# Performance work log

Hardware: AMD Instinct MI355X
Metric: run time of the kernel (lower is better)

## Reference

```python
import jax, jax.numpy as jnp
import numpy as np

B, NPG, DEG = 512, 128, 16          # graphs, nodes/graph, out-degree
N = B * NPG                          # 65536 nodes
E = N * DEG                          # 1048576 edges
IN_DIM, HID, HEADS = 11, 32, 4
K1 = int(np.ceil(0.8 * NPG))         # 103 nodes/graph after pool1
K2 = int(np.ceil(0.8 * K1))          # 83 nodes/graph after pool2


def gat_conv(x, src, dst, mask, W, a_s, a_d, b, n_nodes):
    # PyG GATConv (concat=True, add_self_loops=True, eval mode -> no dropout)
    xp = (x @ W).reshape(n_nodes, HEADS, HID)            # [N,H,C]
    as_ = jnp.einsum('nhc,hc->nh', xp, a_s)
    ad_ = jnp.einsum('nhc,hc->nh', xp, a_d)
    loop = jnp.arange(n_nodes)
    s = jnp.concatenate([src, loop])
    d = jnp.concatenate([dst, loop])
    m = jnp.concatenate([mask, jnp.ones(n_nodes, bool)])
    logit = jax.nn.leaky_relu(as_[s] + ad_[d], 0.2)      # [E+N,H]
    logit = jnp.where(m[:, None], logit, -1e9)
    mx = jax.ops.segment_max(logit, d, num_segments=n_nodes)
    ex = jnp.exp(logit - mx[d]) * m[:, None]
    den = jax.ops.segment_sum(ex, d, num_segments=n_nodes)
    alpha = ex / (den[d] + 1e-16)                        # segment softmax over dst
    out = jax.ops.segment_sum(alpha[:, :, None] * xp[s], d, num_segments=n_nodes)
    return out.reshape(n_nodes, HEADS * HID) + b


def topk_pool(x, src, dst, mask, w, npg, k):
    # PyG TopKPooling: score = tanh((x*w).sum(-1)/||w||); keep top ceil(ratio*n) per graph
    nb = x.shape[0] // npg
    score = jnp.tanh((x @ w) / jnp.linalg.norm(w))
    vals, idx = jax.lax.top_k(score.reshape(nb, npg), k)  # [B,k]
    perm = (idx + (jnp.arange(nb) * npg)[:, None]).reshape(-1)
    x_new = x[perm] * vals.reshape(-1, 1)
    remap = jnp.full(nb * npg, -1).at[perm].set(jnp.arange(nb * k))
    ns, nd = remap[src], remap[dst]
    m = mask & (ns >= 0) & (nd >= 0)
    return x_new, jnp.where(m, ns, 0), jnp.where(m, nd, 0), m


def setup_inputs():
    key = jax.random.key(0)
    ks = jax.random.split(key, 24)
    s = 0.05
    x = jax.random.normal(ks[0], (N, IN_DIM), jnp.float32)
    src = jnp.repeat(jnp.arange(N), DEG)
    dst = (src // NPG) * NPG + jax.random.randint(ks[1], (E,), 0, NPG)
    edge_index = jnp.stack([src, dst])
    edge_attr = jax.random.normal(ks[2], (E, 4), jnp.float32)
    batch = jnp.repeat(jnp.arange(B), NPG)
    p = dict(
        W_g1=jax.random.normal(ks[3], (IN_DIM, HEADS * HID), jnp.float32) * s,
        att_src1=jax.random.normal(ks[4], (HEADS, HID), jnp.float32) * s,
        att_dst1=jax.random.normal(ks[5], (HEADS, HID), jnp.float32) * s,
        b_g1=jnp.zeros((HEADS * HID,), jnp.float32),
        W_t1=jax.random.normal(ks[6], (HEADS * HID, HID), jnp.float32) * s,
        b_t1=jnp.zeros((HID,), jnp.float32),
        pool_w1=jax.random.normal(ks[7], (HID,), jnp.float32) * s,
        W_g2=jax.random.normal(ks[8], (HID, HEADS * HID), jnp.float32) * s,
        att_src2=jax.random.normal(ks[9], (HEADS, HID), jnp.float32) * s,
        att_dst2=jax.random.normal(ks[10], (HEADS, HID), jnp.float32) * s,
        b_g2=jnp.zeros((HEADS * HID,), jnp.float32),
        W_t2=jax.random.normal(ks[11], (HEADS * HID, HID), jnp.float32) * s,
        b_t2=jnp.zeros((HID,), jnp.float32),
        pool_w2=jax.random.normal(ks[12], (HID,), jnp.float32) * s,
        W_l1=jax.random.normal(ks[13], (2 * HID, 256), jnp.float32) * s,
        b_l1=jnp.zeros((256,), jnp.float32),
        W_l2=jax.random.normal(ks[14], (256, 1024), jnp.float32) * s,
        b_l2=jnp.zeros((1024,), jnp.float32),
        W_l3=jax.random.normal(ks[15], (1024, 1), jnp.float32) * s,
        b_l3=jnp.zeros((1,), jnp.float32),
    )
    return dict(x=x, edge_index=edge_index, edge_attr=edge_attr, batch=batch, **p)


def reference(x, edge_index, edge_attr, batch,
              W_g1, att_src1, att_dst1, b_g1, W_t1, b_t1, pool_w1,
              W_g2, att_src2, att_dst2, b_g2, W_t2, b_t2, pool_w2,
              W_l1, b_l1, W_l2, b_l2, W_l3, b_l3):
    # edge_attr is ignored (GATConv built without edge_dim); batch is implicit
    # in the fixed equal-size graph layout.  Eval mode -> dropout disabled.
    src, dst = edge_index[0], edge_index[1]
    mask = jnp.ones(E, bool)
    h = jax.nn.relu(gat_conv(x, src, dst, mask, W_g1, att_src1, att_dst1, b_g1, N))
    h = h @ W_t1 + b_t1
    h, src, dst, mask = topk_pool(h, src, dst, mask, pool_w1, NPG, K1)
    h1 = h.reshape(B, K1, HID)
    g1 = jnp.concatenate([h1.max(1), h1.mean(1)], axis=1)   # [B, 2*HID]
    h = jax.nn.relu(gat_conv(h, src, dst, mask, W_g2, att_src2, att_dst2, b_g2, B * K1))
    h = h @ W_t2 + b_t2
    h, src, dst, mask = topk_pool(h, src, dst, mask, pool_w2, K1, K2)
    h2 = h.reshape(B, K2, HID)
    g2 = jnp.concatenate([h2.max(1), h2.mean(1)], axis=1)
    g = g1 + g2
    g = jax.nn.relu(g @ W_l1 + b_l1)
    g = jax.nn.relu(g @ W_l2 + b_l2)
    return g @ W_l3 + b_l3                                   # [B,1]
```

## Files before the change

kernel.cpp:

```cpp
#include <hip/hip_runtime.h>
#include <math.h>

constexpr int NPGc  = 128;
constexpr int NG    = 512;
constexpr int EPGc  = 2048;
constexpr int ETOT  = 1048576;
constexpr int IND   = 11;
constexpr int HIDc  = 32;
constexpr int FD    = 128;
constexpr int K1c   = 103;
constexpr int K2c   = 83;
constexpr int NN    = NG * NPGc;
constexpr int N2c   = NG * K1c;
constexpr int EPAD  = 2432;
constexpr int SBCAP = 2560;
constexpr int OFFSTR= 264;

__device__ __forceinline__ float lrelu(float x){ return fmaxf(x, 0.2f*x); }

__device__ __forceinline__ void agg4(const float4* __restrict__ X4, int r, int cbase, float e,
                                     float4& A0, float4& A1, float4& A2, float4& A3)
{
    int b = r * 8, s = r & 7;
    float4 u0 = X4[b + ((cbase+0) ^ s)];
    A0.x = fmaf(e, u0.x, A0.x); A0.y = fmaf(e, u0.y, A0.y); A0.z = fmaf(e, u0.z, A0.z); A0.w = fmaf(e, u0.w, A0.w);
    float4 u1 = X4[b + ((cbase+1) ^ s)];
    A1.x = fmaf(e, u1.x, A1.x); A1.y = fmaf(e, u1.y, A1.y); A1.z = fmaf(e, u1.z, A1.z); A1.w = fmaf(e, u1.w, A1.w);
    float4 u2 = X4[b + ((cbase+2) ^ s)];
    A2.x = fmaf(e, u2.x, A2.x); A2.y = fmaf(e, u2.y, A2.y); A2.z = fmaf(e, u2.z, A2.z); A2.w = fmaf(e, u2.w, A2.w);
    float4 u3 = X4[b + ((cbase+3) ^ s)];
    A3.x = fmaf(e, u3.x, A3.x); A3.y = fmaf(e, u3.y, A3.y); A3.z = fmaf(e, u3.z, A3.z); A3.w = fmaf(e, u3.w, A3.w);
}

template<int KIN>
__device__ void foldDev(const float* __restrict__ Wg, const float* __restrict__ avs,
                        const float* __restrict__ avd, float* __restrict__ S, float* __restrict__ D, int t)
{
    if (t < KIN * 4) {
        int k = t >> 2, h = t & 3;
        float s = 0.f, d = 0.f;
        for (int j = 0; j < HIDc; j++) {
            float w = Wg[k*FD + h*HIDc + j];
            s = fmaf(w, avs[h*HIDc + j], s);
            d = fmaf(w, avd[h*HIDc + j], d);
        }
        S[t] = s; D[t] = d;
    }
}

__global__ __launch_bounds__(256) void k_prep(const int* __restrict__ ei,
    const float* __restrict__ W1g, const float* __restrict__ s1, const float* __restrict__ d1,
    const float* __restrict__ W2g, const float* __restrict__ s2, const float* __restrict__ d2,
    int* __restrict__ csrOff, unsigned char* __restrict__ csrSB,
    float* __restrict__ S1, float* __restrict__ D1, float* __restrict__ S2, float* __restrict__ D2)
{
    int b = blockIdx.x, t = threadIdx.x;
    if (b >= NG) {
        if (b == NG)     foldDev<IND>(W1g, s1, d1, S1, D1, t);
        else             foldDev<HIDc>(W2g, s2, d2, S2, D2, t);
        return;
    }
    int g = b;
    __shared__ int cnt[128], cur[128], offL[129];
    __shared__ __align__(16) unsigned char sbL[SBCAP];
    const int FILL1 = (int)0x80808080u;
    if (t < 128) cnt[t] = 0;
    if (t < SBCAP/16) ((int4*)sbL)[t] = make_int4(FILL1, FILL1, FILL1, FILL1);
    __syncthreads();
    const int* dstG = ei + ETOT + g * EPGc;
    int dnv[8];
    #pragma unroll
    for (int q = 0; q < 8; q++) {
        int e = t + 256*q;
        dnv[q] = dstG[e] - g * NPGc;
        atomicAdd(&cnt[dnv[q]], 1);
    }
    __syncthreads();
    if (t < 64) {
        int c0 = cnt[2*t], c1 = cnt[2*t + 1];
        int p0 = (c0 + 3) & ~3, p1 = (c1 + 3) & ~3;
        int ps = p0 + p1, P = ps;
        #pragma unroll
        for (int dl = 1; dl < 64; dl <<= 1) { int v = __shfl_up(P, dl); if (t >= dl) P += v; }
        int E0 = P - ps;
        offL[2*t] = E0; offL[2*t + 1] = E0 + p0;
        cur[2*t]  = E0; cur[2*t + 1]  = E0 + p0;
        if (t == 63) offL[128] = P;
    }
    __syncthreads();
    #pragma unroll
    for (int q = 0; q < 8; q++) {
        int e = t + 256*q;
        int pos = atomicAdd(&cur[dnv[q]], 1);
        sbL[pos] = (unsigned char)(e >> 4);
    }
    __syncthreads();
    if (t < SBCAP/16) ((int4*)(csrSB + (size_t)g * SBCAP))[t] = ((const int4*)sbL)[t];
    if (t <= 128) csrOff[g*OFFSTR + t] = offL[t];
    if (t < 128)  csrOff[g*OFFSTR + 132 + t] = cur[t];
}

template<int NNODE, int KIN>
__global__ __launch_bounds__(256) void k_gat(
    const float* __restrict__ xin, const float* __restrict__ Wg,
    const float* __restrict__ WsS, const float* __restrict__ WsD,
    const int* __restrict__ csrOff, const unsigned char* __restrict__ csrSB,
    const float* __restrict__ bias, const float* __restrict__ Wt,
    float* __restrict__ htp)
{
    int g = blockIdx.x, h = blockIdx.y, t = threadIdx.x;
    __shared__ __align__(16) float xpL[NNODE * 32];
    __shared__ __align__(16) float WL[KIN * 32];
    __shared__ __align__(16) unsigned char sbL[SBCAP];
    __shared__ float asL[NNODE + 1], adL[NNODE];
    __shared__ unsigned short offL[NNODE + 1];

    const float* xg = xin + (size_t)g * NNODE * KIN;

    for (int i = t; i < KIN * 32; i += 256) { int k = i >> 5, c = i & 31; WL[i] = Wg[k*FD + h*32 + c]; }
    if (t <= NNODE) offL[t] = (unsigned short)csrOff[g*OFFSTR + t];
    if (t < SBCAP/16) ((int4*)sbL)[t] = ((const int4*)(csrSB + (size_t)g * SBCAP))[t];
    if (t == 0) asL[NNODE] = -1e30f;
    __syncthreads();

    for (int p = t; p < NNODE * 8; p += 256) {
        int n = p >> 3, c4 = p & 7;
        float4 acc = make_float4(0.f, 0.f, 0.f, 0.f);
        if constexpr ((KIN & 3) == 0) {
            const float4* xr4 = (const float4*)(xg + (size_t)n * KIN);
            #pragma unroll
            for (int k4 = 0; k4 < KIN/4; k4++) {
                float4 xv = xr4[k4];
                float4 w;
                w = *(const float4*)&WL[(k4*4+0)*32 + c4*4];
                acc.x = fmaf(xv.x, w.x, acc.x); acc.y = fmaf(xv.x, w.y, acc.y); acc.z = fmaf(xv.x, w.z, acc.z); acc.w = fmaf(xv.x, w.w, acc.w);
                w = *(const float4*)&WL[(k4*4+1)*32 + c4*4];
                acc.x = fmaf(xv.y, w.x, acc.x); acc.y = fmaf(xv.y, w.y, acc.y); acc.z = fmaf(xv.y, w.z, acc.z); acc.w = fmaf(xv.y, w.w, acc.w);
                w = *(const float4*)&WL[(k4*4+2)*32 + c4*4];
                acc.x = fmaf(xv.z, w.x, acc.x); acc.y = fmaf(xv.z, w.y, acc.y); acc.z = fmaf(xv.z, w.z, acc.z); acc.w = fmaf(xv.z, w.w, acc.w);
                w = *(const float4*)&WL[(k4*4+3)*32 + c4*4];
                acc.x = fmaf(xv.w, w.x, acc.x); acc.y = fmaf(xv.w, w.y, acc.y); acc.z = fmaf(xv.w, w.z, acc.z); acc.w = fmaf(xv.w, w.w, acc.w);
            }
        } else {
            const float* xr = xg + (size_t)n * KIN;
            #pragma unroll
            for (int k = 0; k < KIN; k++) {
                float xv = xr[k];
                float4 w4 = *(const float4*)&WL[k*32 + c4*4];
                acc.x = fmaf(xv, w4.x, acc.x); acc.y = fmaf(xv, w4.y, acc.y);
                acc.z = fmaf(xv, w4.z, acc.z); acc.w = fmaf(xv, w4.w, acc.w);
            }
        }
        ((float4*)xpL)[n*8 + (c4 ^ (n & 7))] = acc;
    }
    if (t < NNODE) {
        const float* xr = xg + (size_t)t * KIN;
        float s = 0.f, d = 0.f;
        #pragma unroll
        for (int k = 0; k < KIN; k++) { float v = xr[k]; s = fmaf(v, WsS[k*4 + h], s); d = fmaf(v, WsD[k*4 + h], d); }
        asL[t] = s; adL[t] = d;
    }
    __syncthreads();

    const float4* X4 = (const float4*)xpL;
    float4 A0, A1, A2, A3;
    int n = 0, cbase = 0;
    bool act = (t < NNODE * 2);
    if (act) {
        n = t >> 1;
        const int half = t & 1;
        cbase = half * 4;
        float as_n = asL[n], adn = adL[n];
        int lo = offL[n], hi = offL[n + 1];
        int mid = lo + (((hi - lo) >> 3) << 2);
        int slo = half ? mid : lo;
        int shi = half ? hi  : mid;
        float mx = -INFINITY;
        for (int i = slo; i < shi; i += 4) {
            unsigned int q4 = *(const unsigned int*)(sbL + i);
            float a0 = asL[q4 & 255], a1 = asL[(q4 >> 8) & 255];
            float a2 = asL[(q4 >> 16) & 255], a3 = asL[q4 >> 24];
            mx = fmaxf(fmaxf(fmaxf(fmaxf(mx, a0), a1), a2), a3);
        }
        mx = fmaxf(mx, __shfl_xor(mx, 1));
        mx = fmaxf(mx, as_n);
        float m = lrelu(mx + adn);
        float den = half ? 0.f : expf(lrelu(as_n + adn) - m);
        for (int i = slo; i < shi; i += 4) {
            unsigned int q4 = *(const unsigned int*)(sbL + i);
            den += expf(lrelu(asL[q4 & 255] + adn) - m);
            den += expf(lrelu(asL[(q4 >> 8) & 255] + adn) - m);
            den += expf(lrelu(asL[(q4 >> 16) & 255] + adn) - m);
            den += expf(lrelu(asL[q4 >> 24] + adn) - m);
        }
        den += __shfl_xor(den, 1);
        float inv = 1.f / (den + 1e-16f);
        float w0 = expf(lrelu(as_n + adn) - m);
        int sw = n & 7, nb = n * 8;
        float4 v0 = X4[nb + ((cbase+0) ^ sw)];
        A0 = make_float4(w0*v0.x, w0*v0.y, w0*v0.z, w0*v0.w);
        float4 v1 = X4[nb + ((cbase+1) ^ sw)];
        A1 = make_float4(w0*v1.x, w0*v1.y, w0*v1.z, w0*v1.w);
        float4 v2 = X4[nb + ((cbase+2) ^ sw)];
        A2 = make_float4(w0*v2.x, w0*v2.y, w0*v2.z, w0*v2.w);
        float4 v3 = X4[nb + ((cbase+3) ^ sw)];
        A3 = make_float4(w0*v3.x, w0*v3.y, w0*v3.z, w0*v3.w);
        for (int s = lo; s < hi; s += 4) {
            unsigned int q4 = *(const unsigned int*)(sbL + s);
            int s0 = q4 & 255, s1 = (q4 >> 8) & 255, s2 = (q4 >> 16) & 255, s3 = q4 >> 24;
            float e0 = expf(lrelu(asL[s0] + adn) - m);
            float e1 = expf(lrelu(asL[s1] + adn) - m);
            float e2 = expf(lrelu(asL[s2] + adn) - m);
            float e3 = expf(lrelu(asL[s3] + adn) - m);
            agg4(X4, min(s0, NNODE-1), cbase, e0, A0, A1, A2, A3);
            agg4(X4, min(s1, NNODE-1), cbase, e1, A0, A1, A2, A3);
            agg4(X4, min(s2, NNODE-1), cbase, e2, A0, A1, A2, A3);
            agg4(X4, min(s3, NNODE-1), cbase, e3, A0, A1, A2, A3);
        }
        const float* bb = bias + h*32 + cbase*4;
        float4 b0 = *(const float4*)(bb);
        float4 b1 = *(const float4*)(bb + 4);
        float4 b2 = *(const float4*)(bb + 8);
        float4 b3 = *(const float4*)(bb + 12);
        A0.x = fmaxf(fmaf(A0.x, inv, b0.x), 0.f); A0.y = fmaxf(fmaf(A0.y, inv, b0.y), 0.f);
        A0.z = fmaxf(fmaf(A0.z, inv, b0.z), 0.f); A0.w = fmaxf(fmaf(A0.w, inv, b0.w), 0.f);
        A1.x = fmaxf(fmaf(A1.x, inv, b1.x), 0.f); A1.y = fmaxf(fmaf(A1.y, inv, b1.y), 0.f);
        A1.z = fmaxf(fmaf(A1.z, inv, b1.z), 0.f); A1.w = fmaxf(fmaf(A1.w, inv, b1.w), 0.f);
        A2.x = fmaxf(fmaf(A2.x, inv, b2.x), 0.f); A2.y = fmaxf(fmaf(A2.y, inv, b2.y), 0.f);
        A2.z = fmaxf(fmaf(A2.z, inv, b2.z), 0.f); A2.w = fmaxf(fmaf(A2.w, inv, b2.w), 0.f);
        A3.x = fmaxf(fmaf(A3.x, inv, b3.x), 0.f); A3.y = fmaxf(fmaf(A3.y, inv, b3.y), 0.f);
        A3.z = fmaxf(fmaf(A3.z, inv, b3.z), 0.f); A3.w = fmaxf(fmaf(A3.w, inv, b3.w), 0.f);
    }
    __syncthreads();
    if (act) {
        float4* X4w = (float4*)xpL;
        int sw = n & 7, nb = n * 8;
        X4w[nb + ((cbase+0) ^ sw)] = A0;
        X4w[nb + ((cbase+1) ^ sw)] = A1;
        X4w[nb + ((cbase+2) ^ sw)] = A2;
        X4w[nb + ((cbase+3) ^ sw)] = A3;
    }
    __syncthreads();

    {
        const int n0 = t >> 3, j4 = t & 7;
        const float* WtH = Wt + h*1024 + j4*4;
        #pragma unroll
        for (int rr = 0; rr < 4; rr++) {
            int nn = n0 + rr*32;
            if (nn < NNODE) {
                float4 acc = make_float4(0.f, 0.f, 0.f, 0.f);
                int sw = nn & 7, nb = nn * 8;
                #pragma unroll
                for (int c4 = 0; c4 < 8; c4++) {
                    float4 xv = X4[nb + (c4 ^ sw)];
                    float4 w;
                    w = *(const float4*)(WtH + (c4*4+0)*32);
                    acc.x = fmaf(xv.x, w.x, acc.x); acc.y = fmaf(xv.x, w.y, acc.y); acc.z = fmaf(xv.x, w.z, acc.z); acc.w = fmaf(xv.x, w.w, acc.w);
                    w = *(const float4*)(WtH + (c4*4+1)*32);
                    acc.x = fmaf(xv.y, w.x, acc.x); acc.y = fmaf(xv.y, w.y, acc.y); acc.z = fmaf(xv.y, w.z, acc.z); acc.w = fmaf(xv.y, w.w, acc.w);
                    w = *(const float4*)(WtH + (c4*4+2)*32);
                    acc.x = fmaf(xv.z, w.x, acc.x); acc.y = fmaf(xv.z, w.y, acc.y); acc.z = fmaf(xv.z, w.z, acc.z); acc.w = fmaf(xv.z, w.w, acc.w);
                    w = *(const float4*)(WtH + (c4*4+3)*32);
                    acc.x = fmaf(xv.w, w.x, acc.x); acc.y = fmaf(xv.w, w.y, acc.y); acc.z = fmaf(xv.w, w.z, acc.z); acc.w = fmaf(xv.w, w.w, acc.w);
                }
                *(float4*)(htp + ((size_t)(g * NNODE + nn) * 4 + h) * 32 + j4 * 4) = acc;
            }
        }
    }
}

template<int NIN, int KEEP, bool FIRST>
__global__ __launch_bounds__(512) void k_linpool(
    const float* __restrict__ htp, const float* __restrict__ bt, const float* __restrict__ pw,
    float* __restrict__ xnew, const int* __restrict__ ei,
    int* __restrict__ csrOffW, unsigned char* __restrict__ sbW,
    float* __restrict__ gfeat, const float* __restrict__ gprev,
    const float* __restrict__ W1, const float* __restrict__ b1,
    const float* __restrict__ W2, const float* __restrict__ b2,
    const float* __restrict__ W3, const float* __restrict__ b3,
    float* __restrict__ outp)
{
    int g = blockIdx.x, t = threadIdx.x;
    __shared__ float htL[NIN * 33];
    __shared__ float scoreL[NIN];
    __shared__ int rnkL[NIN];
    __shared__ int cnt[128], cur[128], offL[129];
    __shared__ __align__(16) unsigned char sbL[SBCAP];
    __shared__ float gvec[64];
    __shared__ float h1L[256], red[512];

    for (int p = t; p < NIN * 8; p += 512) {
        int n = p >> 3, q = p & 7;
        const float4* row = (const float4*)(htp + (size_t)(g * NIN + n) * 128);
        float4 s = ((const float4*)bt)[q];
        float4 p0 = row[q], p1 = row[8 + q], p2 = row[16 + q], p3 = row[24 + q];
        s.x += p0.x; s.y += p0.y; s.z += p0.z; s.w += p0.w;
        s.x += p1.x; s.y += p1.y; s.z += p1.z; s.w += p1.w;
        s.x += p2.x; s.y += p2.y; s.z += p2.z; s.w += p2.w;
        s.x += p3.x; s.y += p3.y; s.z += p3.z; s.w += p3.w;
        float* d = htL + n*33 + q*4;
        d[0] = s.x; d[1] = s.y; d[2] = s.z; d[3] = s.w;
    }
    __syncthreads();

    float nrm; { float ss = 0.f; for (int k = 0; k < HIDc; k++) { float w = pw[k]; ss = fmaf(w, w, ss); } nrm = sqrtf(ss); }
    if (t < NIN) {
        float dot = 0.f;
        #pragma unroll
        for (int k = 0; k < HIDc; k++) dot = fmaf(htL[t*33 + k], pw[k], dot);
        scoreL[t] = tanhf(dot / nrm);
    }
    __syncthreads();
    if (t < NIN) {
        float si = scoreL[t]; int rank = 0;
        #pragma unroll 8
        for (int q = 0; q < NIN; q++) {
            float sj = scoreL[q];
            rank += (sj > si || (sj == si && q < t)) ? 1 : 0;
        }
        rnkL[t] = (rank < KEEP) ? rank : -1;
    }
    __syncthreads();
    if constexpr (FIRST) {
        for (int p = t; p < NIN * 32; p += 512) {
            int n = p >> 5, jj = p & 31;
            int rk = rnkL[n];
            if (rk >= 0) xnew[((size_t)g*KEEP + rk)*HIDc + jj] = htL[n*33 + jj] * scoreL[n];
        }
    }
    if (t < HIDc) {
        float mx = -INFINITY, sm = 0.f;
        #pragma unroll 4
        for (int n = 0; n < NIN; n++) {
            if (rnkL[n] >= 0) { float v = htL[n*33 + t] * scoreL[n]; mx = fmaxf(mx, v); sm += v; }
        }
        float mean = sm / (float)KEEP;
        if constexpr (FIRST) {
            gfeat[(size_t)g*64 + t]      = mx;
            gfeat[(size_t)g*64 + 32 + t] = mean;
        } else {
            gvec[t]      = gprev[(size_t)g*64 + t] + mx;
            gvec[32 + t] = gprev[(size_t)g*64 + 32 + t] + mean;
        }
    }

    if constexpr (FIRST) {
        __syncthreads();
        const int FILL2 = (int)0x67676767u;
        if (t < 128) cnt[t] = 0;
        if (t < SBCAP/16) ((int4*)sbL)[t] = make_int4(FILL2, FILL2, FILL2, FILL2);
        __syncthreads();
        const int* dstG = ei + ETOT + g * EPGc;
        int snv[4], dnv[4];
        #pragma unroll
        for (int q = 0; q < 4; q++) {
            int e = t + 512*q;
            int s = rnkL[e >> 4], d = rnkL[dstG[e] - g * NPGc];
            bool ok = (s >= 0 && d >= 0);
            snv[q] = s; dnv[q] = ok ? d : -1;
            if (ok) atomicAdd(&cnt[d], 1);
        }
        __syncthreads();
        if (t < 64) {
            int c0 = cnt[2*t], c1 = cnt[2*t + 1];
            int p0 = (c0 + 3) & ~3, p1 = (c1 + 3) & ~3;
            int ps = p0 + p1, P = ps;
            #pragma unroll
            for (int dl = 1; dl < 64; dl <<= 1) { int v = __shfl_up(P, dl); if (t >= dl) P += v; }
            int E0 = P - ps;
            offL[2*t] = E0; offL[2*t + 1] = E0 + p0;
            cur[2*t]  = E0; cur[2*t + 1]  = E0 + p0;
            if (t == 63) offL[128] = P;
        }
        __syncthreads();
        #pragma unroll
        for (int q = 0; q < 4; q++) {
            if (dnv[q] >= 0) {
                int pos = atomicAdd(&cur[dnv[q]], 1);
                sbL[pos] = (unsigned char)snv[q];
            }
        }
        __syncthreads();
        if (t < SBCAP/16) ((int4*)(sbW + (size_t)g * SBCAP))[t] = ((const int4*)sbL)[t];
        if (t <= K1c) csrOffW[g*OFFSTR + t] = offL[t];
        if (t < K1c)  csrOffW[g*OFFSTR + 132 + t] = cur[t];
    } else {
        __syncthreads();
        if (t < 256) {
            float a = b1[t];
            #pragma unroll 8
            for (int k = 0; k < 64; k++) a = fmaf(gvec[k], W1[k*256 + t], a);
            h1L[t] = fmaxf(a, 0.f);
        }
        __syncthreads();
        float2 bq = *(const float2*)(b2 + 2*t);
        float c0 = bq.x, c1 = bq.y;
        const float2* w2r = (const float2*)W2 + t;
        #pragma unroll 8
        for (int i = 0; i < 256; i++) {
            float hv = h1L[i];
            float2 w = w2r[(size_t)i * 512];
            c0 = fmaf(hv, w.x, c0);
            c1 = fmaf(hv, w.y, c1);
        }
        float2 w3q = *(const float2*)(W3 + 2*t);
        float p = fmaf(fmaxf(c0, 0.f), w3q.x, fmaxf(c1, 0.f) * w3q.y);
        red[t] = p;
        __syncthreads();
        for (int s = 256; s > 0; s >>= 1) { if (t < s) red[t] += red[t + s]; __syncthreads(); }
        if (t == 0) outp[g] = red[0] + b3[0];
    }
}

extern "C" void kernel_launch(void* const* d_in, const int* in_sizes, int n_in,
                              void* d_out, int out_size, void* d_ws, size_t ws_size,
                              hipStream_t stream)
{
    const float* x    = (const float*)d_in[0];
    const int*   ei   = (const int*)  d_in[1];
    const float* W_g1 = (const float*)d_in[4];
    const float* as1w = (const float*)d_in[5];
    const float* ad1w = (const float*)d_in[6];
    const float* b_g1 = (const float*)d_in[7];
    const float* W_t1 = (const float*)d_in[8];
    const float* b_t1 = (const float*)d_in[9];
    const float* pw1  = (const float*)d_in[10];
    const float* W_g2 = (const float*)d_in[11];
    const float* as2w = (const float*)d_in[12];
    const float* ad2w = (const float*)d_in[13];
    const float* b_g2 = (const float*)d_in[14];
    const float* W_t2 = (const float*)d_in[15];
    const float* b_t2 = (const float*)d_in[16];
    const float* pw2  = (const float*)d_in[17];
    const float* W_l1 = (const float*)d_in[18];
    const float* b_l1 = (const float*)d_in[19];
    const float* W_l2 = (const float*)d_in[20];
    const float* b_l2 = (const float*)d_in[21];
    const float* W_l3 = (const float*)d_in[22];
    const float* b_l3 = (const float*)d_in[23];
    float* out = (float*)d_out;

    char* ws = (char*)d_ws;
    size_t off = 0;
    auto alloc = [&](size_t bytes) -> void* {
        void* p = (void*)(ws + off);
        off += ((bytes + 255) / 256) * 256;
        return p;
    };
    float* htp1  = (float*)alloc((size_t)NN * 128 * 4);
    float* htp2  = (float*)alloc((size_t)N2c * 128 * 4);
    float* x2    = (float*)alloc((size_t)N2c * HIDc * 4);
    float* g1    = (float*)alloc((size_t)NG * 64 * 4);
    float* wsS1  = (float*)alloc(64 * 4);
    float* wsD1  = (float*)alloc(64 * 4);
    float* wsS2  = (float*)alloc(128 * 4);
    float* wsD2  = (float*)alloc(128 * 4);
    int*   off1  = (int*)  alloc((size_t)NG * OFFSTR * 4);
    unsigned char* sb1 = (unsigned char*)alloc((size_t)NG * SBCAP);
    int*   off2  = (int*)  alloc((size_t)NG * OFFSTR * 4);
    unsigned char* sb2 = (unsigned char*)alloc((size_t)NG * SBCAP);

    k_prep<<<NG + 2, 256, 0, stream>>>(ei, W_g1, as1w, ad1w, W_g2, as2w, ad2w,
                                       off1, sb1, wsS1, wsD1, wsS2, wsD2);

    k_gat<NPGc, IND><<<dim3(NG, 4), 256, 0, stream>>>(
        x, W_g1, wsS1, wsD1, off1, sb1, b_g1, W_t1, htp1);

    k_linpool<NPGc, K1c, true><<<NG, 512, 0, stream>>>(
        htp1, b_t1, pw1, x2, ei, off2, sb2, g1, nullptr,
        nullptr, nullptr, nullptr, nullptr, nullptr, nullptr, nullptr);

    k_gat<K1c, HIDc><<<dim3(NG, 4), 256, 0, stream>>>(
        x2, W_g2, wsS2, wsD2, off2, sb2, b_g2, W_t2, htp2);

    k_linpool<K1c, K2c, false><<<NG, 512, 0, stream>>>(
        htp2, b_t2, pw2, nullptr, nullptr, nullptr, nullptr, nullptr, g1,
        W_l1, b_l1, W_l2, b_l2, W_l3, b_l3, out);
}
```

Before: 284.6 us.

## Fuse per-head GAT and linear-pool kernels into one per-graph kernel

Merges the GAT kernel, which used to launch one block per (graph, head) and write per-head partial linear outputs to global memory, with the following top-k pooling kernel. One 256-thread block per graph now loops over all four heads and accumulates the transform output in shared memory. This removes the large htp intermediate buffers and their global round trip. The final MLP moves into a separate kernel that handles two graphs per block and shares W1/W2 loads between them. The cost is four times fewer blocks in the GAT stage with heads processed serially, more shared memory per block, and one more launch for the MLP.

```diff
diff --git a/kernel.cpp b/kernel.cpp
--- a/kernel.cpp
+++ b/kernel.cpp
@@ -100,239 +100,219 @@
     if (t < 128)  csrOff[g*OFFSTR + 132 + t] = cur[t];
 }
 
-template<int NNODE, int KIN>
-__global__ __launch_bounds__(256) void k_gat(
+template<int NNODE, int KIN, bool FIRST>
+__global__ __launch_bounds__(256) void k_fgat(
     const float* __restrict__ xin, const float* __restrict__ Wg,
     const float* __restrict__ WsS, const float* __restrict__ WsD,
     const int* __restrict__ csrOff, const unsigned char* __restrict__ csrSB,
     const float* __restrict__ bias, const float* __restrict__ Wt,
-    float* __restrict__ htp)
-{
-    int g = blockIdx.x, h = blockIdx.y, t = threadIdx.x;
+    const float* __restrict__ bt, const float* __restrict__ pw,
+    float* __restrict__ xnew, const int* __restrict__ ei,
+    int* __restrict__ csrOffW, unsigned char* __restrict__ sbW,
+    float* __restrict__ gfeat, const float* __restrict__ gprev, float* __restrict__ gsum)
+{
+    int g = blockIdx.x, t = threadIdx.x;
     __shared__ __align__(16) float xpL[NNODE * 32];
     __shared__ __align__(16) float WL[KIN * 32];
     __shared__ __align__(16) unsigned char sbL[SBCAP];
     __shared__ float asL[NNODE + 1], adL[NNODE];
     __shared__ unsigned short offL[NNODE + 1];
+    __shared__ float htL[NNODE * 33];
+    __shared__ float scoreL[NNODE];
+    __shared__ int rnkL[NNODE];
+    __shared__ int cnt[128], cur[128], offT[129];
 
     const float* xg = xin + (size_t)g * NNODE * KIN;
 
-    for (int i = t; i < KIN * 32; i += 256) { int k = i >> 5, c = i & 31; WL[i] = Wg[k*FD + h*32 + c]; }
     if (t <= NNODE) offL[t] = (unsigned short)csrOff[g*OFFSTR + t];
     if (t < SBCAP/16) ((int4*)sbL)[t] = ((const int4*)(csrSB + (size_t)g * SBCAP))[t];
     if (t == 0) asL[NNODE] = -1e30f;
-    __syncthreads();
-
-    for (int p = t; p < NNODE * 8; p += 256) {
-        int n = p >> 3, c4 = p & 7;
-        float4 acc = make_float4(0.f, 0.f, 0.f, 0.f);
-        if constexpr ((KIN & 3) == 0) {
-            const float4* xr4 = (const float4*)(xg + (size_t)n * KIN);
-            #pragma unroll
-            for (int k4 = 0; k4 < KIN/4; k4++) {
-                float4 xv = xr4[k4];
-                float4 w;
-                w = *(const float4*)&WL[(k4*4+0)*32 + c4*4];
-                acc.x = fmaf(xv.x, w.x, acc.x); acc.y = fmaf(xv.x, w.y, acc.y); acc.z = fmaf(xv.x, w.z, acc.z); acc.w = fmaf(xv.x, w.w, acc.w);
-                w = *(const float4*)&WL[(k4*4+1)*32 + c4*4];
-                acc.x = fmaf(xv.y, w.x, acc.x); acc.y = fmaf(xv.y, w.y, acc.y); acc.z = fmaf(xv.y, w.z, acc.z); acc.w = fmaf(xv.y, w.w, acc.w);
-                w = *(const float4*)&WL[(k4*4+2)*32 + c4*4];
-                acc.x = fmaf(xv.z, w.x, acc.x); acc.y = fmaf(xv.z, w.y, acc.y); acc.z = fmaf(xv.z, w.z, acc.z); acc.w = fmaf(xv.z, w.w, acc.w);
-                w = *(const float4*)&WL[(k4*4+3)*32 + c4*4];
-                acc.x = fmaf(xv.w, w.x, acc.x); acc.y = fmaf(xv.w, w.y, acc.y); acc.z = fmaf(xv.w, w.z, acc.z); acc.w = fmaf(xv.w, w.w, acc.w);
-            }
-        } else {
-            const float* xr = xg + (size_t)n * KIN;
-            #pragma unroll
-            for (int k = 0; k < KIN; k++) {
-                float xv = xr[k];
-                float4 w4 = *(const float4*)&WL[k*32 + c4*4];
-                acc.x = fmaf(xv, w4.x, acc.x); acc.y = fmaf(xv, w4.y, acc.y);
-                acc.z = fmaf(xv, w4.z, acc.z); acc.w = fmaf(xv, w4.w, acc.w);
-            }
-        }
-        ((float4*)xpL)[n*8 + (c4 ^ (n & 7))] = acc;
-    }
-    if (t < NNODE) {
-        const float* xr = xg + (size_t)t * KIN;
-        float s = 0.f, d = 0.f;
-        #pragma unroll
-        for (int k = 0; k < KIN; k++) { float v = xr[k]; s = fmaf(v, WsS[k*4 + h], s); d = fmaf(v, WsD[k*4 + h], d); }
-        asL[t] = s; adL[t] = d;
-    }
-    __syncthreads();
-
-    const float4* X4 = (const float4*)xpL;
-    float4 A0, A1, A2, A3;
-    int n = 0, cbase = 0;
-    bool act = (t < NNODE * 2);
-    if (act) {
-        n = t >> 1;
-        const int half = t & 1;
-        cbase = half * 4;
-        float as_n = asL[n], adn = adL[n];
-        int lo = offL[n], hi = offL[n + 1];
-        int mid = lo + (((hi - lo) >> 3) << 2);
-        int slo = half ? mid : lo;
-        int shi = half ? hi  : mid;
-        float mx = -INFINITY;
-        for (int i = slo; i < shi; i += 4) {
-            unsigned int q4 = *(const unsigned int*)(sbL + i);
-            float a0 = asL[q4 & 255], a1 = asL[(q4 >> 8) & 255];
-            float a2 = asL[(q4 >> 16) & 255], a3 = asL[q4 >> 24];
-            mx = fmaxf(fmaxf(fmaxf(fmaxf(mx, a0), a1), a2), a3);
-        }
-        mx = fmaxf(mx, __shfl_xor(mx, 1));
-        mx = fmaxf(mx, as_n);
-        float m = lrelu(mx + adn);
-        float den = half ? 0.f : expf(lrelu(as_n + adn) - m);
-        for (int i = slo; i < shi; i += 4) {
-            unsigned int q4 = *(const unsigned int*)(sbL + i);
-            den += expf(lrelu(asL[q4 & 255] + adn) - m);
-            den += expf(lrelu(asL[(q4 >> 8) & 255] + adn) - m);
-            den += expf(lrelu(asL[(q4 >> 16) & 255] + adn) - m);
-            den += expf(lrelu(asL[q4 >> 24] + adn) - m);
-        }
-        den += __shfl_xor(den, 1);
-        float inv = 1.f / (den + 1e-16f);
-        float w0 = expf(lrelu(as_n + adn) - m);
-        int sw = n & 7, nb = n * 8;
-        float4 v0 = X4[nb + ((cbase+0) ^ sw)];
-        A0 = make_float4(w0*v0.x, w0*v0.y, w0*v0.z, w0*v0.w);
-        float4 v1 = X4[nb + ((cbase+1) ^ sw)];
-        A1 = make_float4(w0*v1.x, w0*v1.y, w0*v1.z, w0*v1.w);
-        float4 v2 = X4[nb + ((cbase+2) ^ sw)];
-        A2 = make_float4(w0*v2.x, w0*v2.y, w0*v2.z, w0*v2.w);
-        float4 v3 = X4[nb + ((cbase+3) ^ sw)];
-        A3 = make_float4(w0*v3.x, w0*v3.y, w0*v3.z, w0*v3.w);
-        for (int s = lo; s < hi; s += 4) {
-            unsigned int q4 = *(const unsigned int*)(sbL + s);
-            int s0 = q4 & 255, s1 = (q4 >> 8) & 255, s2 = (q4 >> 16) & 255, s3 = q4 >> 24;
-            float e0 = expf(lrelu(asL[s0] + adn) - m);
-            float e1 = expf(lrelu(asL[s1] + adn) - m);
-            float e2 = expf(lrelu(asL[s2] + adn) - m);
-            float e3 = expf(lrelu(asL[s3] + adn) - m);
-            agg4(X4, min(s0, NNODE-1), cbase, e0, A0, A1, A2, A3);
-            agg4(X4, min(s1, NNODE-1), cbase, e1, A0, A1, A2, A3);
-            agg4(X4, min(s2, NNODE-1), cbase, e2, A0, A1, A2, A3);
-            agg4(X4, min(s3, NNODE-1), cbase, e3, A0, A1, A2, A3);
-        }
-        const float* bb = bias + h*32 + cbase*4;
-        float4 b0 = *(const float4*)(bb);
-        float4 b1 = *(const float4*)(bb + 4);
-        float4 b2 = *(const float4*)(bb + 8);
-        float4 b3 = *(const float4*)(bb + 12);
-        A0.x = fmaxf(fmaf(A0.x, inv, b0.x), 0.f); A0.y = fmaxf(fmaf(A0.y, inv, b0.y), 0.f);
-        A0.z = fmaxf(fmaf(A0.z, inv, b0.z), 0.f); A0.w = fmaxf(fmaf(A0.w, inv, b0.w), 0.f);
-        A1.x = fmaxf(fmaf(A1.x, inv, b1.x), 0.f); A1.y = fmaxf(fmaf(A1.y, inv, b1.y), 0.f);
-        A1.z = fmaxf(fmaf(A1.z, inv, b1.z), 0.f); A1.w = fmaxf(fmaf(A1.w, inv, b1.w), 0.f);
-        A2.x = fmaxf(fmaf(A2.x, inv, b2.x), 0.f); A2.y = fmaxf(fmaf(A2.y, inv, b2.y), 0.f);
-        A2.z = fmaxf(fmaf(A2.z, inv, b2.z), 0.f); A2.w = fmaxf(fmaf(A2.w, inv, b2.w), 0.f);
-        A3.x = fmaxf(fmaf(A3.x, inv, b3.x), 0.f); A3.y = fmaxf(fmaf(A3.y, inv, b3.y), 0.f);
-        A3.z = fmaxf(fmaf(A3.z, inv, b3.z), 0.f); A3.w = fmaxf(fmaf(A3.w, inv, b3.w), 0.f);
-    }
-    __syncthreads();
-    if (act) {
-        float4* X4w = (float4*)xpL;
-        int sw = n & 7, nb = n * 8;
-        X4w[nb + ((cbase+0) ^ sw)] = A0;
-        X4w[nb + ((cbase+1) ^ sw)] = A1;
-        X4w[nb + ((cbase+2) ^ sw)] = A2;
-        X4w[nb + ((cbase+3) ^ sw)] = A3;
-    }
-    __syncthreads();
-
-    {
-        const int n0 = t >> 3, j4 = t & 7;
-        const float* WtH = Wt + h*1024 + j4*4;
-        #pragma unroll
-        for (int rr = 0; rr < 4; rr++) {
-            int nn = n0 + rr*32;
-            if (nn < NNODE) {
-                float4 acc = make_float4(0.f, 0.f, 0.f, 0.f);
-                int sw = nn & 7, nb = nn * 8;
+    for (int p = t; p < NNODE * 32; p += 256) { int n = p >> 5, j = p & 31; htL[n*33 + j] = bt[j]; }
+    __syncthreads();
+
+    for (int h = 0; h < 4; h++) {
+        for (int i = t; i < KIN * 32; i += 256) { int k = i >> 5, c = i & 31; WL[i] = Wg[k*FD + h*32 + c]; }
+        __syncthreads();
+
+        for (int p = t; p < NNODE * 8; p += 256) {
+            int n = p >> 3, c4 = p & 7;
+            float4 acc = make_float4(0.f, 0.f, 0.f, 0.f);
+            if constexpr ((KIN & 3) == 0) {
+                const float4* xr4 = (const float4*)(xg + (size_t)n * KIN);
                 #pragma unroll
-                for (int c4 = 0; c4 < 8; c4++) {
-                    float4 xv = X4[nb + (c4 ^ sw)];
+                for (int k4 = 0; k4 < KIN/4; k4++) {
+                    float4 xv = xr4[k4];
                     float4 w;
-                    w = *(const float4*)(WtH + (c4*4+0)*32);
+                    w = *(const float4*)&WL[(k4*4+0)*32 + c4*4];
                     acc.x = fmaf(xv.x, w.x, acc.x); acc.y = fmaf(xv.x, w.y, acc.y); acc.z = fmaf(xv.x, w.z, acc.z); acc.w = fmaf(xv.x, w.w, acc.w);
-                    w = *(const float4*)(WtH + (c4*4+1)*32);
+                    w = *(const float4*)&WL[(k4*4+1)*32 + c4*4];
                     acc.x = fmaf(xv.y, w.x, acc.x); acc.y = fmaf(xv.y, w.y, acc.y); acc.z = fmaf(xv.y, w.z, acc.z); acc.w = fmaf(xv.y, w.w, acc.w);
-                    w = *(const float4*)(WtH + (c4*4+2)*32);
+                    w = *(const float4*)&WL[(k4*4+2)*32 + c4*4];
                     acc.x = fmaf(xv.z, w.x, acc.x); acc.y = fmaf(xv.z, w.y, acc.y); acc.z = fmaf(xv.z, w.z, acc.z); acc.w = fmaf(xv.z, w.w, acc.w);
-                    w = *(const float4*)(WtH + (c4*4+3)*32);
+                    w = *(const float4*)&WL[(k4*4+3)*32 + c4*4];
                     acc.x = fmaf(xv.w, w.x, acc.x); acc.y = fmaf(xv.w, w.y, acc.y); acc.z = fmaf(xv.w, w.z, acc.z); acc.w = fmaf(xv.w, w.w, acc.w);
                 }
-                *(float4*)(htp + ((size_t)(g * NNODE + nn) * 4 + h) * 32 + j4 * 4) = acc;
-            }
-        }
-    }
-}
-
-template<int NIN, int KEEP, bool FIRST>
-__global__ __launch_bounds__(512) void k_linpool(
-    const float* __restrict__ htp, const float* __restrict__ bt, const float* __restrict__ pw,
-    float* __restrict__ xnew, const int* __restrict__ ei,
-    int* __restrict__ csrOffW, unsigned char* __restrict__ sbW,
-    float* __restrict__ gfeat, const float* __restrict__ gprev,
-    const float* __restrict__ W1, const float* __restrict__ b1,
-    const float* __restrict__ W2, const float* __restrict__ b2,
-    const float* __restrict__ W3, const float* __restrict__ b3,
-    float* __restrict__ outp)
-{
-    int g = blockIdx.x, t = threadIdx.x;
-    __shared__ float htL[NIN * 33];
-    __shared__ float scoreL[NIN];
-    __shared__ int rnkL[NIN];
-    __shared__ int cnt[128], cur[128], offL[129];
-    __shared__ __align__(16) unsigned char sbL[SBCAP];
-    __shared__ float gvec[64];
-    __shared__ float h1L[256], red[512];
-
-    for (int p = t; p < NIN * 8; p += 512) {
-        int n = p >> 3, q = p & 7;
-        const float4* row = (const float4*)(htp + (size_t)(g * NIN + n) * 128);
-        float4 s = ((const float4*)bt)[q];
-        float4 p0 = row[q], p1 = row[8 + q], p2 = row[16 + q], p3 = row[24 + q];
-        s.x += p0.x; s.y += p0.y; s.z += p0.z; s.w += p0.w;
-        s.x += p1.x; s.y += p1.y; s.z += p1.z; s.w += p1.w;
-        s.x += p2.x; s.y += p2.y; s.z += p2.z; s.w += p2.w;
-        s.x += p3.x; s.y += p3.y; s.z += p3.z; s.w += p3.w;
-        float* d = htL + n*33 + q*4;
-        d[0] = s.x; d[1] = s.y; d[2] = s.z; d[3] = s.w;
-    }
-    __syncthreads();
+            } else {
+                const float* xr = xg + (size_t)n * KIN;
+                #pragma unroll
+                for (int k = 0; k < KIN; k++) {
+                    float xv = xr[k];
+                    float4 w4 = *(const float4*)&WL[k*32 + c4*4];
+                    acc.x = fmaf(xv, w4.x, acc.x); acc.y = fmaf(xv, w4.y, acc.y);
+                    acc.z = fmaf(xv, w4.z, acc.z); acc.w = fmaf(xv, w4.w, acc.w);
+                }
+            }
+            ((float4*)xpL)[n*8 + (c4 ^ (n & 7))] = acc;
+        }
+        if (t < NNODE) {
+            const float* xr = xg + (size_t)t * KIN;
+            float s = 0.f, d = 0.f;
+            #pragma unroll
+            for (int k = 0; k < KIN; k++) { float v = xr[k]; s = fmaf(v, WsS[k*4 + h], s); d = fmaf(v, WsD[k*4 + h], d); }
+            asL[t] = s; adL[t] = d;
+        }
+        __syncthreads();
+
+        const float4* X4 = (const float4*)xpL;
+        float4 A0, A1, A2, A3;
+        int n = 0, cbase = 0;
+        bool act = (t < NNODE * 2);
+        if (act) {
+            n = t >> 1;
+            const int half = t & 1;
+            cbase = half * 4;
+            float as_n = asL[n], adn = adL[n];
+            int lo = offL[n], hi = offL[n + 1];
+            int mid = lo + (((hi - lo) >> 3) << 2);
+            int slo = half ? mid : lo;
+            int shi = half ? hi  : mid;
+            float mx = -INFINITY;
+            for (int i = slo; i < shi; i += 4) {
+                unsigned int q4 = *(const unsigned int*)(sbL + i);
+                float a0 = asL[q4 & 255], a1 = asL[(q4 >> 8) & 255];
+                float a2 = asL[(q4 >> 16) & 255], a3 = asL[q4 >> 24];
+                mx = fmaxf(fmaxf(fmaxf(fmaxf(mx, a0), a1), a2), a3);
+            }
+            mx = fmaxf(mx, __shfl_xor(mx, 1));
+            mx = fmaxf(mx, as_n);
+            float m = lrelu(mx + adn);
+            float den = half ? 0.f : expf(lrelu(as_n + adn) - m);
+            for (int i = slo; i < shi; i += 4) {
+                unsigned int q4 = *(const unsigned int*)(sbL + i);
+                den += expf(lrelu(asL[q4 & 255] + adn) - m);
+                den += expf(lrelu(asL[(q4 >> 8) & 255] + adn) - m);
+                den += expf(lrelu(asL[(q4 >> 16) & 255] + adn) - m);
+                den += expf(lrelu(asL[q4 >> 24] + adn) - m);
+            }
+            den += __shfl_xor(den, 1);
+            float inv = 1.f / (den + 1e-16f);
+            float w0 = expf(lrelu(as_n + adn) - m);
+            int sw = n & 7, nb = n * 8;
+            float4 v0 = X4[nb + ((cbase+0) ^ sw)];
+            A0 = make_float4(w0*v0.x, w0*v0.y, w0*v0.z, w0*v0.w);
+            float4 v1 = X4[nb + ((cbase+1) ^ sw)];
+            A1 = make_float4(w0*v1.x, w0*v1.y, w0*v1.z, w0*v1.w);
+            float4 v2 = X4[nb + ((cbase+2) ^ sw)];
+            A2 = make_float4(w0*v2.x, w0*v2.y, w0*v2.z, w0*v2.w);
+            float4 v3 = X4[nb + ((cbase+3) ^ sw)];
+            A3 = make_float4(w0*v3.x, w0*v3.y, w0*v3.z, w0*v3.w);
+            for (int s = lo; s < hi; s += 4) {
+                unsigned int q4 = *(const unsigned int*)(sbL + s);
+                int s0 = q4 & 255, s1 = (q4 >> 8) & 255, s2 = (q4 >> 16) & 255, s3 = q4 >> 24;
+                float e0 = expf(lrelu(asL[s0] + adn) - m);
+                float e1 = expf(lrelu(asL[s1] + adn) - m);
+                float e2 = expf(lrelu(asL[s2] + adn) - m);
+                float e3 = expf(lrelu(asL[s3] + adn) - m);
+                agg4(X4, min(s0, NNODE-1), cbase, e0, A0, A1, A2, A3);
+                agg4(X4, min(s1, NNODE-1), cbase, e1, A0, A1, A2, A3);
+                agg4(X4, min(s2, NNODE-1), cbase, e2, A0, A1, A2, A3);
+                agg4(X4, min(s3, NNODE-1), cbase, e3, A0, A1, A2, A3);
+            }
+            const float* bb = bias + h*32 + cbase*4;
+            float4 b0 = *(const float4*)(bb);
+            float4 b1 = *(const float4*)(bb + 4);
+            float4 b2 = *(const float4*)(bb + 8);
+            float4 b3 = *(const float4*)(bb + 12);
+            A0.x = fmaxf(fmaf(A0.x, inv, b0.x), 0.f); A0.y = fmaxf(fmaf(A0.y, inv, b0.y), 0.f);
+            A0.z = fmaxf(fmaf(A0.z, inv, b0.z), 0.f); A0.w = fmaxf(fmaf(A0.w, inv, b0.w), 0.f);
+            A1.x = fmaxf(fmaf(A1.x, inv, b1.x), 0.f); A1.y = fmaxf(fmaf(A1.y, inv, b1.y), 0.f);
+            A1.z = fmaxf(fmaf(A1.z, inv, b1.z), 0.f); A1.w = fmaxf(fmaf(A1.w, inv, b1.w), 0.f);
+            A2.x = fmaxf(fmaf(A2.x, inv, b2.x), 0.f); A2.y = fmaxf(fmaf(A2.y, inv, b2.y), 0.f);
+            A2.z = fmaxf(fmaf(A2.z, inv, b2.z), 0.f); A2.w = fmaxf(fmaf(A2.w, inv, b2.w), 0.f);
+            A3.x = fmaxf(fmaf(A3.x, inv, b3.x), 0.f); A3.y = fmaxf(fmaf(A3.y, inv, b3.y), 0.f);
+            A3.z = fmaxf(fmaf(A3.z, inv, b3.z), 0.f); A3.w = fmaxf(fmaf(A3.w, inv, b3.w), 0.f);
+        }
+        __syncthreads();
+        if (act) {
+            float4* X4w = (float4*)xpL;
+            int sw = n & 7, nb = n * 8;
+            X4w[nb + ((cbase+0) ^ sw)] = A0;
+            X4w[nb + ((cbase+1) ^ sw)] = A1;
+            X4w[nb + ((cbase+2) ^ sw)] = A2;
+            X4w[nb + ((cbase+3) ^ sw)] = A3;
+        }
+        __syncthreads();
+
+        {
+            const int n0 = t >> 3, j4 = t & 7;
+            const float* WtH = Wt + h*1024 + j4*4;
+            #pragma unroll
+            for (int rr = 0; rr < 4; rr++) {
+                int nn = n0 + rr*32;
+                if (nn < NNODE) {
+                    float4 acc = make_float4(0.f, 0.f, 0.f, 0.f);
+                    int sw = nn & 7, nb = nn * 8;
+                    #pragma unroll
+                    for (int c4 = 0; c4 < 8; c4++) {
+                        float4 xv = X4[nb + (c4 ^ sw)];
+                        float4 w;
+                        w = *(const float4*)(WtH + (c4*4+0)*32);
+                        acc.x = fmaf(xv.x, w.x, acc.x); acc.y = fmaf(xv.x, w.y, acc.y); acc.z = fmaf(xv.x, w.z, acc.z); acc.w = fmaf(xv.x, w.w, acc.w);
+                        w = *(const float4*)(WtH + (c4*4+1)*32);
+                        acc.x = fmaf(xv.y, w.x, acc.x); acc.y = fmaf(xv.y, w.y, acc.y); acc.z = fmaf(xv.y, w.z, acc.z); acc.w = fmaf(xv.y, w.w, acc.w);
+                        w = *(const float4*)(WtH + (c4*4+2)*32);
+                        acc.x = fmaf(xv.z, w.x, acc.x); acc.y = fmaf(xv.z, w.y, acc.y); acc.z = fmaf(xv.z, w.z, acc.z); acc.w = fmaf(xv.z, w.w, acc.w);
+                        w = *(const float4*)(WtH + (c4*4+3)*32);
+                        acc.x = fmaf(xv.w, w.x, acc.x); acc.y = fmaf(xv.w, w.y, acc.y); acc.z = fmaf(xv.w, w.z, acc.z); acc.w = fmaf(xv.w, w.w, acc.w);
+                    }
+                    float* hrow = htL + nn*33 + j4*4;
+                    hrow[0] += acc.x; hrow[1] += acc.y; hrow[2] += acc.z; hrow[3] += acc.w;
+                }
+            }
+        }
+        __syncthreads();
+    }
 
     float nrm; { float ss = 0.f; for (int k = 0; k < HIDc; k++) { float w = pw[k]; ss = fmaf(w, w, ss); } nrm = sqrtf(ss); }
-    if (t < NIN) {
+    if (t < NNODE) {
         float dot = 0.f;
         #pragma unroll
         for (int k = 0; k < HIDc; k++) dot = fmaf(htL[t*33 + k], pw[k], dot);
         scoreL[t] = tanhf(dot / nrm);
     }
     __syncthreads();
-    if (t < NIN) {
+    if (t < NNODE) {
         float si = scoreL[t]; int rank = 0;
         #pragma unroll 8
-        for (int q = 0; q < NIN; q++) {
+        for (int q = 0; q < NNODE; q++) {
             float sj = scoreL[q];
             rank += (sj > si || (sj == si && q < t)) ? 1 : 0;
         }
-        rnkL[t] = (rank < KEEP) ? rank : -1;
+        rnkL[t] = (rank < (FIRST ? K1c : K2c)) ? rank : -1;
     }
     __syncthreads();
     if constexpr (FIRST) {
-        for (int p = t; p < NIN * 32; p += 512) {
+        for (int p = t; p < NNODE * 32; p += 256) {
             int n = p >> 5, jj = p & 31;
             int rk = rnkL[n];
-            if (rk >= 0) xnew[((size_t)g*KEEP + rk)*HIDc + jj] = htL[n*33 + jj] * scoreL[n];
+            if (rk >= 0) xnew[((size_t)g*K1c + rk)*HIDc + jj] = htL[n*33 + jj] * scoreL[n];
         }
     }
     if (t < HIDc) {
+        constexpr int KEEP = FIRST ? K1c : K2c;
         float mx = -INFINITY, sm = 0.f;
         #pragma unroll 4
-        for (int n = 0; n < NIN; n++) {
+        for (int n = 0; n < NNODE; n++) {
             if (rnkL[n] >= 0) { float v = htL[n*33 + t] * scoreL[n]; mx = fmaxf(mx, v); sm += v; }
         }
         float mean = sm / (float)KEEP;
@@ -340,8 +320,8 @@
             gfeat[(size_t)g*64 + t]      = mx;
             gfeat[(size_t)g*64 + 32 + t] = mean;
         } else {
-            gvec[t]      = gprev[(size_t)g*64 + t] + mx;
-            gvec[32 + t] = gprev[(size_t)g*64 + 32 + t] + mean;
+            gsum[(size_t)g*64 + t]      = gprev[(size_t)g*64 + t] + mx;
+            gsum[(size_t)g*64 + 32 + t] = gprev[(size_t)g*64 + 32 + t] + mean;
         }
     }
 
@@ -352,10 +332,10 @@
         if (t < SBCAP/16) ((int4*)sbL)[t] = make_int4(FILL2, FILL2, FILL2, FILL2);
         __syncthreads();
         const int* dstG = ei + ETOT + g * EPGc;
-        int snv[4], dnv[4];
+        int snv[8], dnv[8];
         #pragma unroll
-        for (int q = 0; q < 4; q++) {
-            int e = t + 512*q;
+        for (int q = 0; q < 8; q++) {
+            int e = t + 256*q;
             int s = rnkL[e >> 4], d = rnkL[dstG[e] - g * NPGc];
             bool ok = (s >= 0 && d >= 0);
             snv[q] = s; dnv[q] = ok ? d : -1;
@@ -369,13 +349,13 @@
             #pragma unroll
             for (int dl = 1; dl < 64; dl <<= 1) { int v = __shfl_up(P, dl); if (t >= dl) P += v; }
             int E0 = P - ps;
-            offL[2*t] = E0; offL[2*t + 1] = E0 + p0;
+            offT[2*t] = E0; offT[2*t + 1] = E0 + p0;
             cur[2*t]  = E0; cur[2*t + 1]  = E0 + p0;
-            if (t == 63) offL[128] = P;
+            if (t == 63) offT[128] = P;
         }
         __syncthreads();
         #pragma unroll
-        for (int q = 0; q < 4; q++) {
+        for (int q = 0; q < 8; q++) {
             if (dnv[q] >= 0) {
                 int pos = atomicAdd(&cur[dnv[q]], 1);
                 sbL[pos] = (unsigned char)snv[q];
@@ -383,34 +363,61 @@
         }
         __syncthreads();
         if (t < SBCAP/16) ((int4*)(sbW + (size_t)g * SBCAP))[t] = ((const int4*)sbL)[t];
-        if (t <= K1c) csrOffW[g*OFFSTR + t] = offL[t];
+        if (t <= K1c) csrOffW[g*OFFSTR + t] = offT[t];
         if (t < K1c)  csrOffW[g*OFFSTR + 132 + t] = cur[t];
-    } else {
-        __syncthreads();
-        if (t < 256) {
-            float a = b1[t];
-            #pragma unroll 8
-            for (int k = 0; k < 64; k++) a = fmaf(gvec[k], W1[k*256 + t], a);
-            h1L[t] = fmaxf(a, 0.f);
-        }
-        __syncthreads();
-        float2 bq = *(const float2*)(b2 + 2*t);
-        float c0 = bq.x, c1 = bq.y;
-        const float2* w2r = (const float2*)W2 + t;
+    }
+}
+
+__global__ __launch_bounds__(512) void k_mlp(
+    const float* __restrict__ gsum,
+    const float* __restrict__ W1, const float* __restrict__ b1,
+    const float* __restrict__ W2, const float* __restrict__ b2,
+    const float* __restrict__ W3, const float* __restrict__ b3,
+    float* __restrict__ outp)
+{
+    const int t = threadIdx.x;
+    const int g0 = blockIdx.x * 2;
+    __shared__ float gvec[2][64];
+    __shared__ float h1L[2][256];
+    __shared__ float red[2][512];
+
+    if (t < 128) gvec[t >> 6][t & 63] = gsum[(size_t)(g0 + (t >> 6))*64 + (t & 63)];
+    __syncthreads();
+
+    if (t < 256) {
+        float a0 = b1[t], a1v = b1[t];
         #pragma unroll 8
-        for (int i = 0; i < 256; i++) {
-            float hv = h1L[i];
-            float2 w = w2r[(size_t)i * 512];
-            c0 = fmaf(hv, w.x, c0);
-            c1 = fmaf(hv, w.y, c1);
-        }
-        float2 w3q = *(const float2*)(W3 + 2*t);
-        float p = fmaf(fmaxf(c0, 0.f), w3q.x, fmaxf(c1, 0.f) * w3q.y);
-        red[t] = p;
-        __syncthreads();
-        for (int s = 256; s > 0; s >>= 1) { if (t < s) red[t] += red[t + s]; __syncthreads(); }
-        if (t == 0) outp[g] = red[0] + b3[0];
-    }
+        for (int k = 0; k < 64; k++) {
+            float w = W1[k*256 + t];
+            a0  = fmaf(gvec[0][k], w, a0);
+            a1v = fmaf(gvec[1][k], w, a1v);
+        }
+        h1L[0][t] = fmaxf(a0, 0.f);
+        h1L[1][t] = fmaxf(a1v, 0.f);
+    }
+    __syncthreads();
+    float2 bq = *(const float2*)(b2 + 2*t);
+    float c00 = bq.x, c01 = bq.y;
+    float c10 = bq.x, c11 = bq.y;
+    const float2* w2r = (const float2*)W2 + t;
+    #pragma unroll 8
+    for (int i = 0; i < 256; i++) {
+        float2 w = w2r[(size_t)i * 512];
+        float hv0 = h1L[0][i], hv1 = h1L[1][i];
+        c00 = fmaf(hv0, w.x, c00);
+        c01 = fmaf(hv0, w.y, c01);
+        c10 = fmaf(hv1, w.x, c10);
+        c11 = fmaf(hv1, w.y, c11);
+    }
+    float2 w3q = *(const float2*)(W3 + 2*t);
+    red[0][t] = fmaf(fmaxf(c00, 0.f), w3q.x, fmaxf(c01, 0.f) * w3q.y);
+    red[1][t] = fmaf(fmaxf(c10, 0.f), w3q.x, fmaxf(c11, 0.f) * w3q.y);
+    __syncthreads();
+    for (int s = 256; s > 0; s >>= 1) {
+        if (t < s) { red[0][t] += red[0][t + s]; red[1][t] += red[1][t + s]; }
+        __syncthreads();
+    }
+    if (t == 0) { outp[g0] = red[0][0] + b3[0]; outp[g0 + 1] = red[1][0] + b3[0]; }
 }
 
 extern "C" void kernel_launch(void* const* d_in, const int* in_sizes, int n_in,
@@ -448,10 +455,9 @@
         off += ((bytes + 255) / 256) * 256;
         return p;
     };
-    float* htp1  = (float*)alloc((size_t)NN * 128 * 4);
-    float* htp2  = (float*)alloc((size_t)N2c * 128 * 4);
     float* x2    = (float*)alloc((size_t)N2c * HIDc * 4);
     float* g1    = (float*)alloc((size_t)NG * 64 * 4);
+    float* gsum  = (float*)alloc((size_t)NG * 64 * 4);
     float* wsS1  = (float*)alloc(64 * 4);
     float* wsD1  = (float*)alloc(64 * 4);
     float* wsS2  = (float*)alloc(128 * 4);
@@ -464,17 +470,13 @@
     k_prep<<<NG + 2, 256, 0, stream>>>(ei, W_g1, as1w, ad1w, W_g2, as2w, ad2w,
                                        off1, sb1, wsS1, wsD1, wsS2, wsD2);
 
-    k_gat<NPGc, IND><<<dim3(NG, 4), 256, 0, stream>>>(
-        x, W_g1, wsS1, wsD1, off1, sb1, b_g1, W_t1, htp1);
-
-    k_linpool<NPGc, K1c, true><<<NG, 512, 0, stream>>>(
-        htp1, b_t1, pw1, x2, ei, off2, sb2, g1, nullptr,
-        nullptr, nullptr, nullptr, nullptr, nullptr, nullptr, nullptr);
-
-    k_gat<K1c, HIDc><<<dim3(NG, 4), 256, 0, stream>>>(
-        x2, W_g2, wsS2, wsD2, off2, sb2, b_g2, W_t2, htp2);
-
-    k_linpool<K1c, K2c, false><<<NG, 512, 0, stream>>>(
-        htp2, b_t2, pw2, nullptr, nullptr, nullptr, nullptr, nullptr, g1,
-        W_l1, b_l1, W_l2, b_l2, W_l3, b_l3, out);
-}
+    k_fgat<NPGc, IND, true><<<NG, 256, 0, stream>>>(
+        x, W_g1, wsS1, wsD1, off1, sb1, b_g1, W_t1, b_t1, pw1,
+        x2, ei, off2, sb2, g1, nullptr, nullptr);
+
+    k_fgat<K1c, HIDc, false><<<NG, 256, 0, stream>>>(
+        x2, W_g2, wsS2, wsD2, off2, sb2, b_g2, W_t2, b_t2, pw2,
+        nullptr, nullptr, nullptr, nullptr, nullptr, g1, gsum);
+
+    k_mlp<<<NG/2, 512, 0, stream>>>(gsum, W_l1, b_l1, W_l2, b_l2, W_l3, b_l3, out);
+}
```

Measured after the change: 293.6 us. +3.2%, slower.
